# Kernel tuning notes

Measured on AMD Instinct MI355X. Metric: run time of the kernel, lower is better.

## Reference

```python
import jax, jax.numpy as jnp
import numpy as np

B, L, D = 2, 2048, 1024
H = 16          # num_heads
HD = D // H     # head_dim = 64
NEG_INF = jnp.float32(-1e30)


def setup_inputs() -> dict:
    key = jax.random.key(0)
    ks = jax.random.split(key, 10)
    s = 1.0 / np.sqrt(D)
    return {
        "x": jax.random.normal(ks[0], (B, L, D), dtype=jnp.float32),
        "Wq": jax.random.normal(ks[1], (D, D), dtype=jnp.float32) * s,
        "bq": jnp.zeros((D,), jnp.float32),
        "Wk": jax.random.normal(ks[2], (D, D), dtype=jnp.float32) * s,
        "bk": jnp.zeros((D,), jnp.float32),
        "Wv": jax.random.normal(ks[3], (D, D), dtype=jnp.float32) * s,
        "bv": jnp.zeros((D,), jnp.float32),
        "Wo": jax.random.normal(ks[4], (D, D), dtype=jnp.float32) * s,
        "bo": jnp.zeros((D,), jnp.float32),
        "local_scale": jnp.ones((1,), jnp.float32),
        "global_scale": jnp.ones((1,), jnp.float32),
    }


def reference(x, Wq, bq, Wk, bk, Wv, bv, Wo, bo, local_scale, global_scale):
    # projections -> [B, H, L, HD]
    def proj(W, b):
        return (x @ W + b).reshape(B, L, H, HD).transpose(0, 2, 1, 3)
    Q, K, V = proj(Wq, bq), proj(Wk, bk), proj(Wv, bv)
    lh = H // 2
    inv_sqrt = 1.0 / jnp.sqrt(jnp.float32(HD))

    # local (causal) heads
    scores_l = jnp.einsum("bhqd,bhkd->bhqk", Q[:, :lh], K[:, :lh]) * inv_sqrt
    causal = jnp.tril(jnp.ones((L, L), dtype=bool))  # keep lower triangle
    scores_l = jnp.where(causal, scores_l * local_scale, NEG_INF)
    attn_local = jax.nn.softmax(scores_l, axis=-1)
    out_local = jnp.einsum("bhqk,bhkd->bhqd", attn_local, V[:, :lh])

    # global (full) heads
    scores_g = jnp.einsum("bhqd,bhkd->bhqk", Q[:, lh:], K[:, lh:]) * inv_sqrt
    attn_global = jax.nn.softmax(scores_g * global_scale, axis=-1)
    out_global = jnp.einsum("bhqk,bhkd->bhqd", attn_global, V[:, lh:])

    out = jnp.concatenate([out_local, out_global], axis=1)  # [B,H,L,HD]
    out = out.transpose(0, 2, 1, 3).reshape(B, L, D)
    out = out @ Wo + bo
    return (out, attn_local, attn_global)
```

## Files before the change

### kernel.cpp

```cpp
#include <hip/hip_runtime.h>
#include <hip/hip_bf16.h>

#define B 2
#define L 2048
#define D 1024
#define H 16
#define HD 64
#define LH 8
#define NEG_INF -1e30f

typedef __hip_bfloat16 bf16;
typedef unsigned short ushort_t;
typedef short bf16x8 __attribute__((ext_vector_type(8)));
typedef unsigned short us8 __attribute__((ext_vector_type(8)));
typedef float f32x4 __attribute__((ext_vector_type(4)));

#define MFMA16(a, b, c) __builtin_amdgcn_mfma_f32_16x16x32_bf16((a), (b), (c), 0, 0, 0)

#if defined(__has_builtin)
#if __has_builtin(__builtin_amdgcn_global_load_lds)
#define HAVE_GLOAD_LDS 1
#endif
#endif

template<typename T> struct IsF32;
template<> struct IsF32<float> { static constexpr int value = 1; };
template<> struct IsF32<bf16>  { static constexpr int value = 0; };

__device__ __forceinline__ float ldf(const float* p, size_t i) { return p[i]; }
__device__ __forceinline__ float ldf(const bf16* p, size_t i) { return __bfloat162float(p[i]); }

__device__ __forceinline__ float4 ld4(const float* p, size_t i) {
  return *reinterpret_cast<const float4*>(p + i);
}
__device__ __forceinline__ float4 ld4(const bf16* p, size_t i) {
  ushort4 u = *reinterpret_cast<const ushort4*>(p + i);
  float4 f;
  f.x = __uint_as_float(((unsigned)u.x) << 16);
  f.y = __uint_as_float(((unsigned)u.y) << 16);
  f.z = __uint_as_float(((unsigned)u.z) << 16);
  f.w = __uint_as_float(((unsigned)u.w) << 16);
  return f;
}
__device__ __forceinline__ ushort_t bfh(float v) {
  bf16 h = __float2bfloat16(v);
  return *reinterpret_cast<ushort_t*>(&h);
}
__device__ __forceinline__ float bf2f(ushort_t u) {
  return __uint_as_float(((unsigned)u) << 16);
}
__device__ __forceinline__ void stf(float* p, size_t i, float v) { p[i] = v; }
__device__ __forceinline__ void stf(bf16* p, size_t i, float v) { p[i] = __float2bfloat16(v); }
__device__ __forceinline__ void st4(float* p, size_t i, float4 v) {
  *reinterpret_cast<float4*>(p + i) = v;
}

__device__ __forceinline__ int swz(int row, int slot) {
  return row * 64 + (((slot ^ (row & 7)) & 7) << 3);
}
__device__ __forceinline__ int swzc(int row, int c) {
  return row * 64 + (((((c >> 3) ^ row) & 7) << 3) | (c & 7));
}

#if defined(HAVE_GLOAD_LDS)
__device__ __forceinline__ void gload_lds16(const ushort_t* src, ushort_t* dst) {
  __builtin_amdgcn_global_load_lds(
      (const __attribute__((address_space(1))) unsigned int*)src,
      (__attribute__((address_space(3))) unsigned int*)dst, 16, 0, 0);
}
#endif

__device__ __forceinline__ void stage64(const ushort_t* g, size_t gstride,
                                        ushort_t* lds, int w, int ln) {
  #pragma unroll
  for (int c = 0; c < 2; ++c) {
    const int row = 16 * w + 8 * c + (ln >> 3);
    const int slot = ((ln & 7) ^ row) & 7;
    const ushort_t* src = g + (size_t)row * gstride + slot * 8;
#if defined(HAVE_GLOAD_LDS)
    gload_lds16(src, lds + (size_t)(16 * w + 8 * c) * 64);
#else
    *reinterpret_cast<uint4*>(&lds[row * 64 + (ln & 7) * 8]) =
        *reinterpret_cast<const uint4*>(src);
#endif
  }
}

__device__ __forceinline__ void stage128(const ushort_t* g, ushort_t* lds,
                                         int w, int ln) {
  #pragma unroll
  for (int c = 0; c < 4; ++c) {
    const int row = 32 * w + 8 * c + (ln >> 3);
    const int slot = ((ln & 7) ^ row) & 7;
    const ushort_t* src = g + (size_t)row * 1024 + slot * 8;
#if defined(HAVE_GLOAD_LDS)
    gload_lds16(src, lds + (size_t)(32 * w + 8 * c) * 64);
#else
    *reinterpret_cast<uint4*>(&lds[row * 64 + (ln & 7) * 8]) =
        *reinterpret_cast<const uint4*>(src);
#endif
  }
}

__global__ void detect_dtype_kernel(const unsigned short* __restrict__ x,
                                    int* __restrict__ flag) {
  int bad = 0;
  for (int i = threadIdx.x; i < 1024; i += 64) {
    if (((x[i] >> 7) & 0xFF) >= 170) bad = 1;
  }
  unsigned long long m = __ballot(bad);
  if (threadIdx.x == 0) *flag = (m != 0ULL) ? 1 : 0;
}

__global__ __launch_bounds__(256)
void split_f32_kernel(const int* __restrict__ flag, int want,
                      const float* __restrict__ in,
                      ushort_t* __restrict__ hp, ushort_t* __restrict__ lp, int n4) {
  if (*flag != want) return;
  int i = blockIdx.x * 256 + threadIdx.x;
  const int stride = gridDim.x * 256;
  for (; i < n4; i += stride) {
    float4 v = *reinterpret_cast<const float4*>(in + 4 * (size_t)i);
    ushort4 h, l;
    h.x = bfh(v.x); l.x = bfh(v.x - bf2f(h.x));
    h.y = bfh(v.y); l.y = bfh(v.y - bf2f(h.y));
    h.z = bfh(v.z); l.z = bfh(v.z - bf2f(h.z));
    h.w = bfh(v.w); l.w = bfh(v.w - bf2f(h.w));
    *reinterpret_cast<ushort4*>(hp + 4 * (size_t)i) = h;
    *reinterpret_cast<ushort4*>(lp + 4 * (size_t)i) = l;
  }
}

template<typename T>
__global__ __launch_bounds__(256)
void transW_kernel(const int* __restrict__ flag,
                   const T* __restrict__ W0, const T* __restrict__ W1,
                   const T* __restrict__ W2, const T* __restrict__ W3,
                   ushort_t* __restrict__ base, ushort_t* __restrict__ baseWo,
                   int lo_upto) {
  if (*flag != IsF32<T>::value) return;
  const int z = blockIdx.z;
  const T* W = z == 0 ? W0 : (z == 1 ? W1 : (z == 2 ? W2 : W3));
  ushort_t* hp = (z < 3) ? (base + (size_t)z * 2097152) : baseWo;
  ushort_t* lp = hp + 1048576;
  const bool wl_ = IsF32<T>::value && (z < lo_upto);
  __shared__ float ts[64][69];
  const int k0 = blockIdx.x * 64, n0 = blockIdx.y * 64;
  const int t = threadIdx.x;
  #pragma unroll
  for (int p = 0; p < 4; ++p) {
    int r = p * 16 + (t >> 4);
    int c = (t & 15) * 4;
    float4 v = ld4(W, (size_t)(k0 + r) * D + n0 + c);
    ts[r][c] = v.x; ts[r][c + 1] = v.y; ts[r][c + 2] = v.z; ts[r][c + 3] = v.w;
  }
  __syncthreads();
  #pragma unroll
  for (int p = 0; p < 4; ++p) {
    int n = p * 16 + (t >> 4);
    int k4 = (t & 15) * 4;
    ushort4 h, l;
    float a0 = ts[k4][n], a1 = ts[k4 + 1][n], a2 = ts[k4 + 2][n], a3 = ts[k4 + 3][n];
    h.x = bfh(a0); l.x = bfh(a0 - bf2f(h.x));
    h.y = bfh(a1); l.y = bfh(a1 - bf2f(h.y));
    h.z = bfh(a2); l.z = bfh(a2 - bf2f(h.z));
    h.w = bfh(a3); l.w = bfh(a3 - bf2f(h.w));
    size_t o = (size_t)(n0 + n) * D + k0 + k4;
    *reinterpret_cast<ushort4*>(hp + o) = h;
    if (wl_) *reinterpret_cast<ushort4*>(lp + o) = l;
  }
}

template<typename T, int NSA>
__global__ __launch_bounds__(256, 2)
void gemm_kernel(const int* __restrict__ flag,
                 const ushort_t* __restrict__ xA, const ushort_t* __restrict__ xAl,
                 const ushort_t* __restrict__ aoh,
                 const ushort_t* __restrict__ wbase, const ushort_t* __restrict__ woT,
                 const T* __restrict__ bq, const T* __restrict__ bk,
                 const T* __restrict__ bv, const T* __restrict__ bo,
                 ushort_t* __restrict__ qh, ushort_t* __restrict__ ql,
                 ushort_t* __restrict__ kh, ushort_t* __restrict__ kl,
                 ushort_t* __restrict__ vth, T* __restrict__ out0, int zbase) {
  if (*flag != IsF32<T>::value) return;
  const int cpx = gridDim.x >> 3;
  const int swzid = ((int)blockIdx.x & 7) * cpx + ((int)blockIdx.x >> 3);
  const int mtile = swzid & 31;
  const int rest = swzid >> 5;
  const int ntile = rest & 7;
  const int z = zbase + (rest >> 3);
  const int m0 = mtile * 128, n0 = ntile * 128;

  const bool isOut = (z == 3);
  const ushort_t* Ah = isOut ? aoh : xA;
  const ushort_t* wh = isOut ? woT : (wbase + (size_t)z * 2097152);
  const ushort_t* wl = wh + 1048576;
  const bool full = (NSA == 2) && (z < 2);

  __shared__ ushort_t AsH[8192], AsL[8192], BsH[8192], BsL[8192];

  const int ln = threadIdx.x & 63, w = threadIdx.x >> 6;
  const int m = ln & 15, hi = ln >> 4;
  const int wr = w >> 1, wc = w & 1;

  f32x4 acc[4][4] = {};

  for (int k0 = 0; k0 < 1024; k0 += 64) {
    stage128(Ah + (size_t)m0 * 1024 + k0, AsH, w, ln);
    stage128(wh + (size_t)n0 * 1024 + k0, BsH, w, ln);
    if (full) {
      stage128(xAl + (size_t)m0 * 1024 + k0, AsL, w, ln);
      stage128(wl + (size_t)n0 * 1024 + k0, BsL, w, ln);
    }
    __syncthreads();
    #pragma unroll
    for (int kc = 0; kc < 2; ++kc) {
      bf16x8 a_h[4], b_h[4];
      #pragma unroll
      for (int f = 0; f < 4; ++f) {
        a_h[f] = *reinterpret_cast<const bf16x8*>(&AsH[swz(wr * 64 + f * 16 + m, kc * 4 + hi)]);
        b_h[f] = *reinterpret_cast<const bf16x8*>(&BsH[swz(wc * 64 + f * 16 + m, kc * 4 + hi)]);
      }
      #pragma unroll
      for (int fr = 0; fr < 4; ++fr)
        #pragma unroll
        for (int fc = 0; fc < 4; ++fc)
          acc[fr][fc] = MFMA16(a_h[fr], b_h[fc], acc[fr][fc]);
      if (full) {
        bf16x8 a_l[4], b_l[4];
        #pragma unroll
        for (int f = 0; f < 4; ++f) {
          a_l[f] = *reinterpret_cast<const bf16x8*>(&AsL[swz(wr * 64 + f * 16 + m, kc * 4 + hi)]);
          b_l[f] = *reinterpret_cast<const bf16x8*>(&BsL[swz(wc * 64 + f * 16 + m, kc * 4 + hi)]);
        }
        #pragma unroll
        for (int fr = 0; fr < 4; ++fr)
          #pragma unroll
          for (int fc = 0; fc < 4; ++fc) {
            acc[fr][fc] = MFMA16(a_h[fr], b_l[fc], acc[fr][fc]);
            acc[fr][fc] = MFMA16(a_l[fr], b_h[fc], acc[fr][fc]);
          }
      }
    }
    __syncthreads();
  }

  #pragma unroll
  for (int fc = 0; fc < 4; ++fc) {
    const int col = n0 + wc * 64 + fc * 16 + m;
    if (isOut) {
      const float bv_ = ldf(bo, (size_t)col);
      #pragma unroll
      for (int fr = 0; fr < 4; ++fr)
        #pragma unroll
        for (int r = 0; r < 4; ++r) {
          const int tok = m0 + wr * 64 + fr * 16 + 4 * hi + r;
          stf(out0, (size_t)tok * D + col, acc[fr][fc][r] + bv_);
        }
    } else if (z == 2) {
      const int hh = col >> 6, d = col & 63;
      const float bv_ = ldf(bv, (size_t)col);
      #pragma unroll
      for (int fr = 0; fr < 4; ++fr) {
        const int tok0 = m0 + wr * 64 + fr * 16 + 4 * hi;
        const int bb = tok0 >> 11, ll = tok0 & (L - 1);
        ushort4 hv;
        hv.x = bfh(acc[fr][fc][0] + bv_);
        hv.y = bfh(acc[fr][fc][1] + bv_);
        hv.z = bfh(acc[fr][fc][2] + bv_);
        hv.w = bfh(acc[fr][fc][3] + bv_);
        *reinterpret_cast<ushort4*>(
            &vth[((size_t)(bb * H + hh) * HD + d) * L + ll]) = hv;
      }
    } else {
      const int hh = col >> 6, d = col & 63;
      const float bv_ = ldf(z == 0 ? bq : bk, (size_t)col);
      ushort_t* oh = z == 0 ? qh : kh;
      ushort_t* ol = z == 0 ? ql : kl;
      #pragma unroll
      for (int fr = 0; fr < 4; ++fr)
        #pragma unroll
        for (int r = 0; r < 4; ++r) {
          const int tok = m0 + wr * 64 + fr * 16 + 4 * hi + r;
          const int bb = tok >> 11, ll = tok & (L - 1);
          const float v = acc[fr][fc][r] + bv_;
          const size_t o = ((size_t)(bb * H + hh) * L + ll) * HD + d;
          const ushort_t hu = bfh(v);
          oh[o] = hu; ol[o] = bfh(v - bf2f(hu));
        }
    }
  }
}

template<typename T>
__global__ __launch_bounds__(256)
void attn_kernel(const int* __restrict__ flag,
                 const ushort_t* __restrict__ Qh_g, const ushort_t* __restrict__ Ql_g,
                 const ushort_t* __restrict__ Kh_g, const ushort_t* __restrict__ Kl_g,
                 const ushort_t* __restrict__ Vth_g,
                 const T* __restrict__ lsp, const T* __restrict__ gsp,
                 T* __restrict__ attn_l, T* __restrict__ attn_g,
                 ushort_t* __restrict__ AOh) {
  if (*flag != IsF32<T>::value) return;
  const int bid = blockIdx.x;
  const int xcd = bid & 7, slot = bid >> 3;
  const int bhg = xcd + 8 * (slot >> 5);
  const int strip_raw = slot & 31;
  const int bb = bhg >> 4, h = bhg & 15;
  const bool is_local = h < LH;
  const int strip = is_local ? (31 - strip_raw) : strip_raw;
  const int q0 = strip * 64;
  const int ln = threadIdx.x & 63, w = threadIdx.x >> 6;
  const int m = ln & 15, hi = ln >> 4;

  const float cscale =
      (is_local ? ldf(lsp, (size_t)0) : ldf(gsp, (size_t)0)) * 0.125f;
  const size_t bh_off = ((size_t)bb * H + h) * L * HD;
  const ushort_t* Qhb = Qh_g + bh_off;
  const ushort_t* Qlb = Ql_g + bh_off;
  const ushort_t* Khb = Kh_g + bh_off;
  const ushort_t* Klb = Kl_g + bh_off;
  const ushort_t* Vhb = Vth_g + bh_off;

  __shared__ ushort_t KsH[4096], KsL[4096], VsH[4096], Ps[4096];

  bf16x8 qfh[2], qfl[2];
  {
    const size_t qb = (size_t)(q0 + 16 * w + m) * HD + hi * 8;
    qfh[0] = *reinterpret_cast<const bf16x8*>(Qhb + qb);
    qfh[1] = *reinterpret_cast<const bf16x8*>(Qhb + qb + 32);
    qfl[0] = *reinterpret_cast<const bf16x8*>(Qlb + qb);
    qfl[1] = *reinterpret_cast<const bf16x8*>(Qlb + qb + 32);
  }

  float m_ = NEG_INF, l_ = 0.f;
  const int nkt = is_local ? (strip + 1) : (L / 64);
  T* aout = is_local ? attn_l : attn_g;
  const size_t arow0 =
      ((size_t)(bb * LH + (is_local ? h : h - LH)) * L + q0) * L;

  for (int kt = 0; kt < nkt; ++kt) {
    stage64(Khb + (size_t)(kt * 64) * HD, HD, KsH, w, ln);
    __syncthreads();

    f32x4 s[4] = {};
    __builtin_amdgcn_s_setprio(1);
    #pragma unroll
    for (int nt = 0; nt < 4; ++nt) {
      #pragma unroll
      for (int kc = 0; kc < 2; ++kc) {
        bf16x8 kbh = *reinterpret_cast<const bf16x8*>(&KsH[swz(nt * 16 + m, kc * 4 + hi)]);
        s[nt] = MFMA16(kbh, qfh[kc], s[nt]);
      }
    }
    __builtin_amdgcn_s_setprio(0);

    const bool dg = is_local && (kt == strip);
    #pragma unroll
    for (int nt = 0; nt < 4; ++nt)
      #pragma unroll
      for (int r = 0; r < 4; ++r) {
        float v = s[nt][r] * cscale;
        if (dg && (nt * 16 + 4 * hi + r > 16 * w + m)) v = NEG_INF;
        s[nt][r] = v;
      }

    float tm = NEG_INF;
    #pragma unroll
    for (int nt = 0; nt < 4; ++nt)
      #pragma unroll
      for (int r = 0; r < 4; ++r) tm = fmaxf(tm, s[nt][r]);
    tm = fmaxf(tm, __shfl_xor(tm, 16, 64));
    tm = fmaxf(tm, __shfl_xor(tm, 32, 64));
    const float mn = fmaxf(m_, tm);
    float sum = 0.f;
    #pragma unroll
    for (int nt = 0; nt < 4; ++nt)
      #pragma unroll
      for (int r = 0; r < 4; ++r) sum += __expf(s[nt][r] - mn);
    sum += __shfl_xor(sum, 16, 64);
    sum += __shfl_xor(sum, 32, 64);
    l_ = l_ * __expf(m_ - mn) + sum;
    m_ = mn;
    __syncthreads();
  }

  const float invl = 1.0f / l_;
  f32x4 o_[4] = {};

  for (int kt = 0; kt < nkt; ++kt) {
    stage64(Khb + (size_t)(kt * 64) * HD, HD, KsH, w, ln);
    stage64(Klb + (size_t)(kt * 64) * HD, HD, KsL, w, ln);
    stage64(Vhb + (size_t)(kt * 64), L, VsH, w, ln);
    __syncthreads();

    f32x4 s[4] = {};
    __builtin_amdgcn_s_setprio(1);
    #pragma unroll
    for (int nt = 0; nt < 4; ++nt) {
      #pragma unroll
      for (int kc = 0; kc < 2; ++kc) {
        bf16x8 kbh = *reinterpret_cast<const bf16x8*>(&KsH[swz(nt * 16 + m, kc * 4 + hi)]);
        bf16x8 kbl = *reinterpret_cast<const bf16x8*>(&KsL[swz(nt * 16 + m, kc * 4 + hi)]);
        s[nt] = MFMA16(kbh, qfh[kc], s[nt]);
        s[nt] = MFMA16(kbl, qfh[kc], s[nt]);
        s[nt] = MFMA16(kbh, qfl[kc], s[nt]);
      }
    }
    __builtin_amdgcn_s_setprio(0);

    const bool dg = is_local && (kt == strip);
    #pragma unroll
    for (int nt = 0; nt < 4; ++nt) {
      float v0 = s[nt][0] * cscale, v1 = s[nt][1] * cscale;
      float v2 = s[nt][2] * cscale, v3 = s[nt][3] * cscale;
      if (dg) {
        const int kbq = nt * 16 + 4 * hi, qq = 16 * w + m;
        if (kbq + 0 > qq) v0 = NEG_INF;
        if (kbq + 1 > qq) v1 = NEG_INF;
        if (kbq + 2 > qq) v2 = NEG_INF;
        if (kbq + 3 > qq) v3 = NEG_INF;
      }
      ushort4 pk;
      pk.x = bfh(__expf(v0 - m_) * invl);
      pk.y = bfh(__expf(v1 - m_) * invl);
      pk.z = bfh(__expf(v2 - m_) * invl);
      pk.w = bfh(__expf(v3 - m_) * invl);
      *reinterpret_cast<ushort4*>(&Ps[swzc(16 * w + m, nt * 16 + 4 * hi)]) = pk;
    }

    __builtin_amdgcn_s_setprio(1);
    bf16x8 pf0 = *reinterpret_cast<const bf16x8*>(&Ps[swz(16 * w + m, hi)]);
    bf16x8 pf1 = *reinterpret_cast<const bf16x8*>(&Ps[swz(16 * w + m, 4 + hi)]);
    #pragma unroll
    for (int dt = 0; dt < 4; ++dt) {
      bf16x8 vf0 = *reinterpret_cast<const bf16x8*>(&VsH[swz(dt * 16 + m, hi)]);
      bf16x8 vf1 = *reinterpret_cast<const bf16x8*>(&VsH[swz(dt * 16 + m, 4 + hi)]);
      o_[dt] = MFMA16(pf0, vf0, o_[dt]);
      o_[dt] = MFMA16(pf1, vf1, o_[dt]);
    }
    __builtin_amdgcn_s_setprio(0);

    {
      const int pr = 16 * w + (ln >> 2);
      const int cs = (ln & 3) * 2;
      us8 v0 = *reinterpret_cast<const us8*>(&Ps[swz(pr, cs)]);
      us8 v1 = *reinterpret_cast<const us8*>(&Ps[swz(pr, cs + 1)]);
      const size_t gi = arow0 + (size_t)pr * L + (size_t)(kt * 64 + (ln & 3) * 16);
      if constexpr (IsF32<T>::value) {
        float* dst = (float*)aout + gi;
        *reinterpret_cast<float4*>(dst + 0) =
            make_float4(bf2f(v0[0]), bf2f(v0[1]), bf2f(v0[2]), bf2f(v0[3]));
        *reinterpret_cast<float4*>(dst + 4) =
            make_float4(bf2f(v0[4]), bf2f(v0[5]), bf2f(v0[6]), bf2f(v0[7]));
        *reinterpret_cast<float4*>(dst + 8) =
            make_float4(bf2f(v1[0]), bf2f(v1[1]), bf2f(v1[2]), bf2f(v1[3]));
        *reinterpret_cast<float4*>(dst + 12) =
            make_float4(bf2f(v1[4]), bf2f(v1[5]), bf2f(v1[6]), bf2f(v1[7]));
      } else {
        bf16* dst = (bf16*)aout + gi;
        *reinterpret_cast<uint4*>(dst + 0) = *reinterpret_cast<const uint4*>(&v0);
        *reinterpret_cast<uint4*>(dst + 8) = *reinterpret_cast<const uint4*>(&v1);
      }
    }
    __syncthreads();
  }

  if (is_local) {
    const int pr = 16 * w + (ln >> 2);
    const size_t rbase = arow0 + (size_t)pr * L;
    for (int c = nkt * 64 + (ln & 3) * 16; c < L; c += 64) {
      if constexpr (IsF32<T>::value) {
        float* dst = (float*)aout + rbase + c;
        const float4 z4 = make_float4(0.f, 0.f, 0.f, 0.f);
        *reinterpret_cast<float4*>(dst + 0) = z4;
        *reinterpret_cast<float4*>(dst + 4) = z4;
        *reinterpret_cast<float4*>(dst + 8) = z4;
        *reinterpret_cast<float4*>(dst + 12) = z4;
      } else {
        bf16* dst = (bf16*)aout + rbase + c;
        const uint4 z4 = make_uint4(0u, 0u, 0u, 0u);
        *reinterpret_cast<uint4*>(dst + 0) = z4;
        *reinterpret_cast<uint4*>(dst + 8) = z4;
      }
    }
  }

  #pragma unroll
  for (int dt = 0; dt < 4; ++dt)
    #pragma unroll
    for (int r = 0; r < 4; ++r)
      AOh[((size_t)bb * L + q0 + 16 * w + 4 * hi + r) * D + h * HD + dt * 16 + m] =
          bfh(o_[dt][r]);
}

template<typename T>
static void launch_path(void* const* d_in, void* d_out, void* d_ws, hipStream_t stream) {
  const int want = IsF32<T>::value;
  const int* flag = (const int*)d_ws;
  ushort_t* Qh  = (ushort_t*)((char*)d_ws + 256);
  ushort_t* Ql  = Qh + 4194304;
  ushort_t* Kh  = Ql + 4194304;
  ushort_t* Kl  = Kh + 4194304;
  ushort_t* Vth = Kl + 4194304;
  ushort_t* AOh = Vth + 4194304;
  ushort_t* Woth = AOh + 4194304;

  const T* x  = (const T*)d_in[0];
  const T* Wq = (const T*)d_in[1];
  const T* bq = (const T*)d_in[2];
  const T* Wk = (const T*)d_in[3];
  const T* bk = (const T*)d_in[4];
  const T* Wv = (const T*)d_in[5];
  const T* bv = (const T*)d_in[6];
  const T* Wo = (const T*)d_in[7];
  const T* bo = (const T*)d_in[8];
  const T* ls = (const T*)d_in[9];
  const T* gs = (const T*)d_in[10];

  T* out0   = (T*)d_out;
  T* attn_l = out0 + (size_t)B * L * D;
  T* attn_g = attn_l + (size_t)B * LH * L * L;
  ushort_t* xh  = (ushort_t*)attn_g;
  ushort_t* xl  = xh + 4194304;
  ushort_t* Wt3 = xh + 8388608;

  constexpr int NSA = IsF32<T>::value ? 2 : 1;

  if constexpr (IsF32<T>::value)
    split_f32_kernel<<<1024, 256, 0, stream>>>(flag, want, (const float*)x, xh, xl, 1048576);
  transW_kernel<T><<<dim3(16, 16, 4), 256, 0, stream>>>(
      flag, Wq, Wk, Wv, Wo, Wt3, Woth, 2);
  const ushort_t* xA = IsF32<T>::value ? xh : (const ushort_t*)x;
  gemm_kernel<T, NSA><<<768, 256, 0, stream>>>(
      flag, xA, xl, AOh, Wt3, Woth, bq, bk, bv, bo,
      Qh, Ql, Kh, Kl, Vth, out0, 0);
  attn_kernel<T><<<1024, 256, 0, stream>>>(
      flag, Qh, Ql, Kh, Kl, Vth, ls, gs, attn_l, attn_g, AOh);
  gemm_kernel<T, NSA><<<256, 256, 0, stream>>>(
      flag, xA, xl, AOh, Wt3, Woth, bq, bk, bv, bo,
      Qh, Ql, Kh, Kl, Vth, out0, 3);
}

extern "C" void kernel_launch(void* const* d_in, const int* in_sizes, int n_in,
                              void* d_out, int out_size, void* d_ws, size_t ws_size,
                              hipStream_t stream) {
  int* flag = (int*)d_ws;
  detect_dtype_kernel<<<1, 64, 0, stream>>>((const unsigned short*)d_in[0], flag);
  launch_path<float>(d_in, d_out, d_ws, stream);
  launch_path<bf16>(d_in, d_out, d_ws, stream);
}
```

Measured before the change: 972.0 us.

## Double-buffer attention K/V staging and retile projection GEMMs to 128x64

The attention kernel now keeps two LDS buffers for K-high, K-low and V. The next key tile is staged while the current one is computed, which removes one barrier per iteration and hides global-load latency. The GEMM uses a 128x64 tile with each wave owning 32 rows. A compile-time FULL flag sizes LDS and launch bounds, so the split-precision Q/K projections and the single-precision V/output projections run as separate launches with more resident blocks. The risks are larger LDS use in attention and the correctness of buffer reuse, which depends on the barrier left at the end of each loop iteration.

```diff
diff --git a/kernel.cpp b/kernel.cpp
--- a/kernel.cpp
+++ b/kernel.cpp
@@ -51,9 +51,6 @@
 }
 __device__ __forceinline__ void stf(float* p, size_t i, float v) { p[i] = v; }
 __device__ __forceinline__ void stf(bf16* p, size_t i, float v) { p[i] = __float2bfloat16(v); }
-__device__ __forceinline__ void st4(float* p, size_t i, float4 v) {
-  *reinterpret_cast<float4*>(p + i) = v;
-}
 
 __device__ __forceinline__ int swz(int row, int slot) {
   return row * 64 + (((slot ^ (row & 7)) & 7) << 3);
@@ -171,8 +168,8 @@
   }
 }
 
-template<typename T, int NSA>
-__global__ __launch_bounds__(256, 2)
+template<typename T, int NSA, bool FULL>
+__global__ __launch_bounds__(256, FULL ? 3 : 4)
 void gemm_kernel(const int* __restrict__ flag,
                  const ushort_t* __restrict__ xA, const ushort_t* __restrict__ xAl,
                  const ushort_t* __restrict__ aoh,
@@ -181,60 +178,64 @@
                  const T* __restrict__ bv, const T* __restrict__ bo,
                  ushort_t* __restrict__ qh, ushort_t* __restrict__ ql,
                  ushort_t* __restrict__ kh, ushort_t* __restrict__ kl,
-                 ushort_t* __restrict__ vth, T* __restrict__ out0, int zbase) {
+                 ushort_t* __restrict__ vth, T* __restrict__ out0, int zfix) {
   if (*flag != IsF32<T>::value) return;
   const int cpx = gridDim.x >> 3;
   const int swzid = ((int)blockIdx.x & 7) * cpx + ((int)blockIdx.x >> 3);
   const int mtile = swzid & 31;
-  const int rest = swzid >> 5;
-  const int ntile = rest & 7;
-  const int z = zbase + (rest >> 3);
-  const int m0 = mtile * 128, n0 = ntile * 128;
+  const int ntile = (swzid >> 5) & 15;
+  const int z = (zfix >= 0) ? zfix : (swzid >> 9);
+  const int m0 = mtile * 128, n0 = ntile * 64;
 
   const bool isOut = (z == 3);
   const ushort_t* Ah = isOut ? aoh : xA;
   const ushort_t* wh = isOut ? woT : (wbase + (size_t)z * 2097152);
   const ushort_t* wl = wh + 1048576;
-  const bool full = (NSA == 2) && (z < 2);
-
-  __shared__ ushort_t AsH[8192], AsL[8192], BsH[8192], BsL[8192];
+
+  constexpr int LDSUS = FULL ? 24576 : 12288;
+  __shared__ ushort_t lds[LDSUS];
+  ushort_t* AsH = lds;
+  ushort_t* BsH = lds + 8192;
+  ushort_t* AsL = FULL ? (lds + 12288) : nullptr;
+  ushort_t* BsL = FULL ? (lds + 20480) : nullptr;
 
   const int ln = threadIdx.x & 63, w = threadIdx.x >> 6;
   const int m = ln & 15, hi = ln >> 4;
-  const int wr = w >> 1, wc = w & 1;
-
-  f32x4 acc[4][4] = {};
+
+  f32x4 acc[2][4] = {};
 
   for (int k0 = 0; k0 < 1024; k0 += 64) {
     stage128(Ah + (size_t)m0 * 1024 + k0, AsH, w, ln);
-    stage128(wh + (size_t)n0 * 1024 + k0, BsH, w, ln);
-    if (full) {
+    stage64(wh + (size_t)n0 * 1024 + k0, 1024, BsH, w, ln);
+    if constexpr (FULL) {
       stage128(xAl + (size_t)m0 * 1024 + k0, AsL, w, ln);
-      stage128(wl + (size_t)n0 * 1024 + k0, BsL, w, ln);
+      stage64(wl + (size_t)n0 * 1024 + k0, 1024, BsL, w, ln);
     }
     __syncthreads();
     #pragma unroll
     for (int kc = 0; kc < 2; ++kc) {
-      bf16x8 a_h[4], b_h[4];
-      #pragma unroll
-      for (int f = 0; f < 4; ++f) {
-        a_h[f] = *reinterpret_cast<const bf16x8*>(&AsH[swz(wr * 64 + f * 16 + m, kc * 4 + hi)]);
-        b_h[f] = *reinterpret_cast<const bf16x8*>(&BsH[swz(wc * 64 + f * 16 + m, kc * 4 + hi)]);
-      }
-      #pragma unroll
-      for (int fr = 0; fr < 4; ++fr)
+      bf16x8 a_h[2], b_h[4];
+      #pragma unroll
+      for (int f = 0; f < 2; ++f)
+        a_h[f] = *reinterpret_cast<const bf16x8*>(&AsH[swz(w * 32 + f * 16 + m, kc * 4 + hi)]);
+      #pragma unroll
+      for (int f = 0; f < 4; ++f)
+        b_h[f] = *reinterpret_cast<const bf16x8*>(&BsH[swz(f * 16 + m, kc * 4 + hi)]);
+      #pragma unroll
+      for (int fr = 0; fr < 2; ++fr)
         #pragma unroll
         for (int fc = 0; fc < 4; ++fc)
           acc[fr][fc] = MFMA16(a_h[fr], b_h[fc], acc[fr][fc]);
-      if (full) {
-        bf16x8 a_l[4], b_l[4];
+      if constexpr (FULL) {
+        bf16x8 a_l[2], b_l[4];
         #pragma unroll
-        for (int f = 0; f < 4; ++f) {
-          a_l[f] = *reinterpret_cast<const bf16x8*>(&AsL[swz(wr * 64 + f * 16 + m, kc * 4 + hi)]);
-          b_l[f] = *reinterpret_cast<const bf16x8*>(&BsL[swz(wc * 64 + f * 16 + m, kc * 4 + hi)]);
-        }
+        for (int f = 0; f < 2; ++f)
+          a_l[f] = *reinterpret_cast<const bf16x8*>(&AsL[swz(w * 32 + f * 16 + m, kc * 4 + hi)]);
         #pragma unroll
-        for (int fr = 0; fr < 4; ++fr)
+        for (int f = 0; f < 4; ++f)
+          b_l[f] = *reinterpret_cast<const bf16x8*>(&BsL[swz(f * 16 + m, kc * 4 + hi)]);
+        #pragma unroll
+        for (int fr = 0; fr < 2; ++fr)
           #pragma unroll
           for (int fc = 0; fc < 4; ++fc) {
             acc[fr][fc] = MFMA16(a_h[fr], b_l[fc], acc[fr][fc]);
@@ -247,22 +248,22 @@
 
   #pragma unroll
   for (int fc = 0; fc < 4; ++fc) {
-    const int col = n0 + wc * 64 + fc * 16 + m;
+    const int col = n0 + fc * 16 + m;
     if (isOut) {
       const float bv_ = ldf(bo, (size_t)col);
       #pragma unroll
-      for (int fr = 0; fr < 4; ++fr)
+      for (int fr = 0; fr < 2; ++fr)
         #pragma unroll
         for (int r = 0; r < 4; ++r) {
-          const int tok = m0 + wr * 64 + fr * 16 + 4 * hi + r;
+          const int tok = m0 + w * 32 + fr * 16 + 4 * hi + r;
           stf(out0, (size_t)tok * D + col, acc[fr][fc][r] + bv_);
         }
     } else if (z == 2) {
       const int hh = col >> 6, d = col & 63;
       const float bv_ = ldf(bv, (size_t)col);
       #pragma unroll
-      for (int fr = 0; fr < 4; ++fr) {
-        const int tok0 = m0 + wr * 64 + fr * 16 + 4 * hi;
+      for (int fr = 0; fr < 2; ++fr) {
+        const int tok0 = m0 + w * 32 + fr * 16 + 4 * hi;
         const int bb = tok0 >> 11, ll = tok0 & (L - 1);
         ushort4 hv;
         hv.x = bfh(acc[fr][fc][0] + bv_);
@@ -278,10 +279,10 @@
       ushort_t* oh = z == 0 ? qh : kh;
       ushort_t* ol = z == 0 ? ql : kl;
       #pragma unroll
-      for (int fr = 0; fr < 4; ++fr)
+      for (int fr = 0; fr < 2; ++fr)
         #pragma unroll
         for (int r = 0; r < 4; ++r) {
-          const int tok = m0 + wr * 64 + fr * 16 + 4 * hi + r;
+          const int tok = m0 + w * 32 + fr * 16 + 4 * hi + r;
           const int bb = tok >> 11, ll = tok & (L - 1);
           const float v = acc[fr][fc][r] + bv_;
           const size_t o = ((size_t)(bb * H + hh) * L + ll) * HD + d;
@@ -293,7 +294,7 @@
 }
 
 template<typename T>
-__global__ __launch_bounds__(256)
+__global__ __launch_bounds__(256, 2)
 void attn_kernel(const int* __restrict__ flag,
                  const ushort_t* __restrict__ Qh_g, const ushort_t* __restrict__ Ql_g,
                  const ushort_t* __restrict__ Kh_g, const ushort_t* __restrict__ Kl_g,
@@ -322,7 +323,7 @@
   const ushort_t* Klb = Kl_g + bh_off;
   const ushort_t* Vhb = Vth_g + bh_off;
 
-  __shared__ ushort_t KsH[4096], KsL[4096], VsH[4096], Ps[4096];
+  __shared__ ushort_t KsH[2][4096], KsL[2][4096], VsH[2][4096], Ps[4096];
 
   bf16x8 qfh[2], qfl[2];
   {
@@ -339,9 +340,12 @@
   const size_t arow0 =
       ((size_t)(bb * LH + (is_local ? h : h - LH)) * L + q0) * L;
 
+  stage64(Khb, HD, KsH[0], w, ln);
+  __syncthreads();
   for (int kt = 0; kt < nkt; ++kt) {
-    stage64(Khb + (size_t)(kt * 64) * HD, HD, KsH, w, ln);
-    __syncthreads();
+    const int cur = kt & 1;
+    if (kt + 1 < nkt)
+      stage64(Khb + (size_t)((kt + 1) * 64) * HD, HD, KsH[cur ^ 1], w, ln);
 
     f32x4 s[4] = {};
     __builtin_amdgcn_s_setprio(1);
@@ -349,7 +353,7 @@
     for (int nt = 0; nt < 4; ++nt) {
       #pragma unroll
       for (int kc = 0; kc < 2; ++kc) {
-        bf16x8 kbh = *reinterpret_cast<const bf16x8*>(&KsH[swz(nt * 16 + m, kc * 4 + hi)]);
+        bf16x8 kbh = *reinterpret_cast<const bf16x8*>(&KsH[cur][swz(nt * 16 + m, kc * 4 + hi)]);
         s[nt] = MFMA16(kbh, qfh[kc], s[nt]);
       }
     }
@@ -388,11 +392,17 @@
   const float invl = 1.0f / l_;
   f32x4 o_[4] = {};
 
+  stage64(Khb, HD, KsH[0], w, ln);
+  stage64(Klb, HD, KsL[0], w, ln);
+  stage64(Vhb, L, VsH[0], w, ln);
+  __syncthreads();
   for (int kt = 0; kt < nkt; ++kt) {
-    stage64(Khb + (size_t)(kt * 64) * HD, HD, KsH, w, ln);
-    stage64(Klb + (size_t)(kt * 64) * HD, HD, KsL, w, ln);
-    stage64(Vhb + (size_t)(kt * 64), L, VsH, w, ln);
-    __syncthreads();
+    const int cur = kt & 1;
+    if (kt + 1 < nkt) {
+      stage64(Khb + (size_t)((kt + 1) * 64) * HD, HD, KsH[cur ^ 1], w, ln);
+      stage64(Klb + (size_t)((kt + 1) * 64) * HD, HD, KsL[cur ^ 1], w, ln);
+      stage64(Vhb + (size_t)((kt + 1) * 64), L, VsH[cur ^ 1], w, ln);
+    }
 
     f32x4 s[4] = {};
     __builtin_amdgcn_s_setprio(1);
@@ -400,8 +410,8 @@
     for (int nt = 0; nt < 4; ++nt) {
       #pragma unroll
       for (int kc = 0; kc < 2; ++kc) {
-        bf16x8 kbh = *reinterpret_cast<const bf16x8*>(&KsH[swz(nt * 16 + m, kc * 4 + hi)]);
-        bf16x8 kbl = *reinterpret_cast<const bf16x8*>(&KsL[swz(nt * 16 + m, kc * 4 + hi)]);
+        bf16x8 kbh = *reinterpret_cast<const bf16x8*>(&KsH[cur][swz(nt * 16 + m, kc * 4 + hi)]);
+        bf16x8 kbl = *reinterpret_cast<const bf16x8*>(&KsL[cur][swz(nt * 16 + m, kc * 4 + hi)]);
         s[nt] = MFMA16(kbh, qfh[kc], s[nt]);
         s[nt] = MFMA16(kbl, qfh[kc], s[nt]);
         s[nt] = MFMA16(kbh, qfl[kc], s[nt]);
@@ -434,8 +444,8 @@
     bf16x8 pf1 = *reinterpret_cast<const bf16x8*>(&Ps[swz(16 * w + m, 4 + hi)]);
     #pragma unroll
     for (int dt = 0; dt < 4; ++dt) {
-      bf16x8 vf0 = *reinterpret_cast<const bf16x8*>(&VsH[swz(dt * 16 + m, hi)]);
-      bf16x8 vf1 = *reinterpret_cast<const bf16x8*>(&VsH[swz(dt * 16 + m, 4 + hi)]);
+      bf16x8 vf0 = *reinterpret_cast<const bf16x8*>(&VsH[cur][swz(dt * 16 + m, hi)]);
+      bf16x8 vf1 = *reinterpret_cast<const bf16x8*>(&VsH[cur][swz(dt * 16 + m, 4 + hi)]);
       o_[dt] = MFMA16(pf0, vf0, o_[dt]);
       o_[dt] = MFMA16(pf1, vf1, o_[dt]);
     }
@@ -532,12 +542,22 @@
   transW_kernel<T><<<dim3(16, 16, 4), 256, 0, stream>>>(
       flag, Wq, Wk, Wv, Wo, Wt3, Woth, 2);
   const ushort_t* xA = IsF32<T>::value ? xh : (const ushort_t*)x;
-  gemm_kernel<T, NSA><<<768, 256, 0, stream>>>(
-      flag, xA, xl, AOh, Wt3, Woth, bq, bk, bv, bo,
-      Qh, Ql, Kh, Kl, Vth, out0, 0);
+
+  if constexpr (IsF32<T>::value) {
+    gemm_kernel<T, NSA, true><<<1024, 256, 0, stream>>>(
+        flag, xA, xl, AOh, Wt3, Woth, bq, bk, bv, bo,
+        Qh, Ql, Kh, Kl, Vth, out0, -1);
+    gemm_kernel<T, NSA, false><<<512, 256, 0, stream>>>(
+        flag, xA, xl, AOh, Wt3, Woth, bq, bk, bv, bo,
+        Qh, Ql, Kh, Kl, Vth, out0, 2);
+  } else {
+    gemm_kernel<T, NSA, false><<<1536, 256, 0, stream>>>(
+        flag, xA, xl, AOh, Wt3, Woth, bq, bk, bv, bo,
+        Qh, Ql, Kh, Kl, Vth, out0, -1);
+  }
   attn_kernel<T><<<1024, 256, 0, stream>>>(
       flag, Qh, Ql, Kh, Kl, Vth, ls, gs, attn_l, attn_g, AOh);
-  gemm_kernel<T, NSA><<<256, 256, 0, stream>>>(
+  gemm_kernel<T, NSA, false><<<512, 256, 0, stream>>>(
       flag, xA, xl, AOh, Wt3, Woth, bq, bk, bv, bo,
       Qh, Ql, Kh, Kl, Vth, out0, 3);
 }
```

New measurement: 966.9 us. No clear change (-0.5%).
